# Optimization experiments

Measured on AMD Instinct MI355X. Metric: run time of the kernel, lower is better.

The kernel has to match this reference:

```python
import jax, jax.numpy as jnp
import numpy as np

N_NODES = 32768
N_EDGES = 524288
N_FEAT = 256
HID = 256
N_GRAPHS = 64
N_CLASSES = 4
NODES_PER_GRAPH = N_NODES // N_GRAPHS
BN_EPS = 1e-5


def setup_inputs() -> dict:
    key = jax.random.key(0)
    ks = jax.random.split(key, 16)
    x = jax.random.normal(ks[0], (N_NODES, N_FEAT), dtype=jnp.float32)
    edge_index = jax.random.randint(ks[1], (2, N_EDGES), 0, N_NODES, dtype=jnp.int32)
    batch = (jnp.arange(N_NODES, dtype=jnp.int32) // NODES_PER_GRAPH)
    def xavier(k, shape):
        fan_in, fan_out = shape[0], shape[1]
        a = float(np.sqrt(6.0 / (fan_in + fan_out)))
        return jax.random.uniform(k, shape, jnp.float32, -a, a)
    return {
        "x": x, "edge_index": edge_index, "batch": batch,
        "W1": xavier(ks[2], (N_FEAT, HID)), "b1": jnp.zeros((HID,), jnp.float32),
        "g1": jnp.ones((HID,), jnp.float32), "be1": jnp.zeros((HID,), jnp.float32),
        "W2": xavier(ks[3], (HID, HID)), "b2": jnp.zeros((HID,), jnp.float32),
        "g2": jnp.ones((HID,), jnp.float32), "be2": jnp.zeros((HID,), jnp.float32),
        "W_ih": xavier(ks[4], (HID, 4 * HID)), "W_hh": xavier(ks[5], (HID, 4 * HID)),
        "b_ih": jnp.zeros((4 * HID,), jnp.float32), "b_hh": jnp.zeros((4 * HID,), jnp.float32),
        "W_fc": xavier(ks[6], (HID, N_CLASSES)), "b_fc": jnp.zeros((N_CLASSES,), jnp.float32),
    }


def gcn_conv(x, W, b, src, dst):
    # PyG GCNConv: add self-loops, symmetric normalization, aggregate, then bias
    h = x @ W                                   # [N, H]
    deg = jnp.zeros((x.shape[0],), h.dtype).at[dst].add(1.0) + 1.0  # in-deg + self-loop
    dinv = jax.lax.rsqrt(deg)
    coef = dinv[src] * dinv[dst]                # [E]
    msg = h[src] * coef[:, None]                # gather + scale, [E, H]
    agg = jnp.zeros_like(h).at[dst].add(msg)    # scatter-add
    agg = agg + h * (1.0 / deg)[:, None]        # self-loop term (norm = 1/deg)
    return agg + b


def batch_norm(x, gamma, beta):
    mean = jnp.mean(x, axis=0)
    var = jnp.mean(jnp.square(x - mean), axis=0)  # biased, as torch BN training
    return (x - mean) * jax.lax.rsqrt(var + BN_EPS) * gamma + beta


def reference(x, edge_index, batch, W1, b1, g1, be1, W2, b2, g2, be2,
              W_ih, W_hh, b_ih, b_hh, W_fc, b_fc):
    src, dst = edge_index[0], edge_index[1]
    h = jax.nn.relu(batch_norm(gcn_conv(x, W1, b1, src, dst), g1, be1))
    h = jax.nn.relu(batch_norm(gcn_conv(h, W2, b2, src, dst), g2, be2))
    # global mean pool over graphs
    sums = jax.ops.segment_sum(h, batch, num_segments=N_GRAPHS)
    cnts = jax.ops.segment_sum(jnp.ones((h.shape[0],), h.dtype), batch, num_segments=N_GRAPHS)
    pooled = sums / cnts[:, None]               # [G, H]
    # LSTM, seq_len = 1, zero initial state -> single cell step
    h0 = jnp.zeros((N_GRAPHS, HID), h.dtype)
    c0 = jnp.zeros((N_GRAPHS, HID), h.dtype)
    gates = pooled @ W_ih + h0 @ W_hh + b_ih + b_hh  # [G, 4H]
    i, f, g, o = jnp.split(gates, 4, axis=1)
    c1 = jax.nn.sigmoid(f) * c0 + jax.nn.sigmoid(i) * jnp.tanh(g)
    h1 = jax.nn.sigmoid(o) * jnp.tanh(c1)
    logits = h1 @ W_fc + b_fc
    logp = jax.nn.log_softmax(logits, axis=1)
    return (logp, (h1[None], c1[None]))
```

## Files before the change

### kernel.cpp

```cpp
#include <hip/hip_runtime.h>
#include <math.h>

#define N_NODES 32768
#define N_FEAT 256
#define HID 256
#define N_GRAPHS 64
#define NPG 512
#define N_CLASSES 4
#define BN_EPS 1e-5f

typedef __attribute__((ext_vector_type(8))) short bf16x8;
typedef __attribute__((ext_vector_type(4))) float f32x4;

__device__ __forceinline__ ushort f2b(float f) {
    union { float f; uint u; } v; v.f = f;
    uint u = v.u;
    return (ushort)((u + 0x7FFFu + ((u >> 16) & 1u)) >> 16);
}
__device__ __forceinline__ float bf2f(ushort u) {
    union { uint u; float f; } v; v.u = ((uint)u) << 16;
    return v.f;
}

__global__ void k_count(const int* __restrict__ dst, int* __restrict__ degcnt, int E) {
    int e = blockIdx.x * 256 + threadIdx.x;
    if (e < E) atomicAdd(&degcnt[dst[e]], 1);
}

__global__ __launch_bounds__(1024) void k_scan_all(const int* __restrict__ degcnt,
                                                   float* __restrict__ dinv,
                                                   int* __restrict__ row_start,
                                                   int* __restrict__ cursor) {
    __shared__ int wsum[16];
    int t = threadIdx.x;
    int base = t * 32;
    int s = 0;
#pragma unroll
    for (int i = 0; i < 32; ++i) s += degcnt[base + i];
    int lane = t & 63, w = t >> 6;
    int v = s;
    for (int off = 1; off < 64; off <<= 1) {
        int u = __shfl_up(v, off);
        if (lane >= off) v += u;
    }
    if (lane == 63) wsum[w] = v;
    __syncthreads();
    if (t < 16) {
        int x = wsum[t];
        for (int off = 1; off < 16; off <<= 1) {
            int u = __shfl_up(x, off, 16);
            if (t >= off) x += u;
        }
        wsum[t] = x;
    }
    __syncthreads();
    int run = ((w > 0) ? wsum[w - 1] : 0) + v - s;
    for (int i = 0; i < 32; ++i) {
        int n = base + i;
        int c = degcnt[n];
        row_start[n] = run;
        cursor[n] = run;
        dinv[n] = rsqrtf((float)(c + 1));
        run += c;
    }
}

__global__ void k_fill(const int* __restrict__ src, const int* __restrict__ dst,
                       const float* __restrict__ dinv, int* __restrict__ cursor,
                       uint2* __restrict__ csr, int E) {
    int e = blockIdx.x * 256 + threadIdx.x;
    if (e >= E) return;
    int d = dst[e], s = src[e];
    float coef = dinv[s] * dinv[d];
    int pos = atomicAdd(&cursor[d], 1);
    csr[pos] = make_uint2((uint)s, __float_as_uint(coef));
}

__global__ void k_prep(const float* __restrict__ x, ushort* __restrict__ xb, int n8blk,
                       const float* __restrict__ W1, const float* __restrict__ W2,
                       ushort* __restrict__ Wt1, ushort* __restrict__ Wt2) {
    int b = blockIdx.x;
    if (b < n8blk) {
        int i = b * 256 + threadIdx.x;
        float4 v0 = *(const float4*)(x + (size_t)i * 8);
        float4 v1 = *(const float4*)(x + (size_t)i * 8 + 4);
        uint4 o;
        o.x = (uint)f2b(v0.x) | ((uint)f2b(v0.y) << 16);
        o.y = (uint)f2b(v0.z) | ((uint)f2b(v0.w) << 16);
        o.z = (uint)f2b(v1.x) | ((uint)f2b(v1.y) << 16);
        o.w = (uint)f2b(v1.z) | ((uint)f2b(v1.w) << 16);
        *(uint4*)(xb + (size_t)i * 8) = o;
    } else {
        int wb = b - n8blk;
        const float* W = (wb < 256) ? W1 : W2;
        ushort* Wt = (wb < 256) ? Wt1 : Wt2;
        int n = wb & 255;
        int k = threadIdx.x;
        Wt[n * 256 + k] = f2b(W[k * 256 + n]);
    }
}

__global__ __launch_bounds__(256) void k_gemm_bf16(const ushort* __restrict__ A,
                                                   const ushort* __restrict__ Bt,
                                                   ushort* __restrict__ hs) {
    int wid = threadIdx.x >> 6;
    int lane = threadIdx.x & 63;
    int m0 = blockIdx.y * 256 + wid * 64;
    int n0 = blockIdx.x * 64;
    int r = lane & 15;
    int ko = (lane >> 4) * 8;

    const ushort* Ab = A + (size_t)(m0 + r) * 256 + ko;
    const ushort* Bb = Bt + (size_t)(n0 + r) * 256 + ko;

    f32x4 acc[4][4] = {};
#pragma unroll
    for (int ks = 0; ks < 8; ++ks) {
        bf16x8 a[4], b[4];
#pragma unroll
        for (int i = 0; i < 4; ++i) {
            a[i] = *(const bf16x8*)(Ab + i * (16 * 256) + ks * 32);
            b[i] = *(const bf16x8*)(Bb + i * (16 * 256) + ks * 32);
        }
#pragma unroll
        for (int i = 0; i < 4; ++i)
#pragma unroll
            for (int j = 0; j < 4; ++j)
                acc[i][j] = __builtin_amdgcn_mfma_f32_16x16x32_bf16(a[i], b[j], acc[i][j], 0, 0, 0);
    }

    int rr = (lane >> 4) * 4;
    int cc = lane & 15;
#pragma unroll
    for (int i = 0; i < 4; ++i) {
        int row = m0 + i * 16 + rr;
#pragma unroll
        for (int j = 0; j < 4; ++j) {
            int col = n0 + j * 16 + cc;
            int slice = col >> 5;
            int within = col & 31;
            ushort* dstp = hs + (size_t)slice * (N_NODES * 32) + (size_t)row * 32 + within;
#pragma unroll
            for (int r2 = 0; r2 < 4; ++r2)
                dstp[(size_t)r2 * 32] = f2b(acc[i][j][r2]);
        }
    }
}

__global__ __launch_bounds__(256) void k_agg_bn(const ushort* __restrict__ hs,
                                                const uint2* __restrict__ csr,
                                                const int* __restrict__ row_start,
                                                const int* __restrict__ degcnt,
                                                const float* __restrict__ dinv,
                                                const float* __restrict__ bias,
                                                float* __restrict__ agg,
                                                float* __restrict__ bnsum,
                                                float* __restrict__ bnsq) {
    int slice = blockIdx.x & 7;
    int grp = blockIdx.x >> 3;
    int wid = threadIdx.x >> 6;
    int lane = threadIdx.x & 63;
    int j4 = lane >> 4;
    int fp = lane & 15;
    const ushort* hS = hs + (size_t)slice * (N_NODES * 32);

    float b0 = 0.f, b1v = 0.f;
    if (j4 == 0) {
        b0 = bias[slice * 32 + fp * 2];
        b1v = bias[slice * 32 + fp * 2 + 1];
    }

    float s0 = 0.f, q0 = 0.f, s1 = 0.f, q1 = 0.f;

    for (int t = 0; t < 8; ++t) {
        int n = grp * 32 + wid * 8 + t;
        int base = row_start[n];
        int cnt = degcnt[n];
        float ax = 0.f, ay = 0.f;
        if (j4 == 0) {
            float dv = dinv[n];
            uint hv = *(const uint*)(hS + (size_t)n * 32 + fp * 2);
            float inv = dv * dv;
            ax = bf2f((ushort)hv) * inv + b0;
            ay = bf2f((ushort)(hv >> 16)) * inv + b1v;
        }
        int j = j4;
        for (; j + 4 < cnt; j += 8) {
            uint2 e0 = csr[base + j];
            uint2 e1 = csr[base + j + 4];
            float c0 = __uint_as_float(e0.y);
            float c1 = __uint_as_float(e1.y);
            uint h0 = *(const uint*)(hS + (size_t)e0.x * 32 + fp * 2);
            uint h1 = *(const uint*)(hS + (size_t)e1.x * 32 + fp * 2);
            ax += c0 * bf2f((ushort)h0) + c1 * bf2f((ushort)h1);
            ay += c0 * bf2f((ushort)(h0 >> 16)) + c1 * bf2f((ushort)(h1 >> 16));
        }
        if (j < cnt) {
            uint2 e0 = csr[base + j];
            float c0 = __uint_as_float(e0.y);
            uint h0 = *(const uint*)(hS + (size_t)e0.x * 32 + fp * 2);
            ax += c0 * bf2f((ushort)h0);
            ay += c0 * bf2f((ushort)(h0 >> 16));
        }
        ax += __shfl_xor(ax, 16); ay += __shfl_xor(ay, 16);
        ax += __shfl_xor(ax, 32); ay += __shfl_xor(ay, 32);
        if (j4 == 0) {
            *(float2*)&agg[(size_t)n * HID + slice * 32 + fp * 2] = make_float2(ax, ay);
            s0 += ax; q0 += ax * ax; s1 += ay; q1 += ay * ay;
        }
    }

    __shared__ float ls[4][16][4];
    if (j4 == 0) {
        ls[wid][fp][0] = s0; ls[wid][fp][1] = q0;
        ls[wid][fp][2] = s1; ls[wid][fp][3] = q1;
    }
    __syncthreads();
    if (threadIdx.x < 64) {
        int f = threadIdx.x >> 2, v = threadIdx.x & 3;
        float tsum = ls[0][f][v] + ls[1][f][v] + ls[2][f][v] + ls[3][f][v];
        int feat = slice * 32 + f * 2 + (v >> 1);
        if ((v & 1) == 0) atomicAdd(&bnsum[feat], tsum);
        else              atomicAdd(&bnsq[feat], tsum);
    }
}

__global__ void k_bn_apply_b(const float* __restrict__ x, const float* __restrict__ bnsum,
                             const float* __restrict__ bnsq, const float* __restrict__ gamma,
                             const float* __restrict__ beta, ushort* __restrict__ out) {
    int i = blockIdx.x * 256 + threadIdx.x;
    if (i >= N_NODES * HID / 4) return;
    int f = (i & 63) * 4;
    const float invN = 1.0f / (float)N_NODES;
    float4 v = *(const float4*)(x + (size_t)i * 4);
    float r[4];
    float vv[4] = {v.x, v.y, v.z, v.w};
#pragma unroll
    for (int q = 0; q < 4; ++q) {
        float mean = bnsum[f + q] * invN;
        float var = bnsq[f + q] * invN - mean * mean;
        float t = (vv[q] - mean) * rsqrtf(var + BN_EPS) * gamma[f + q] + beta[f + q];
        r[q] = t > 0.0f ? t : 0.0f;
    }
    uint2 o;
    o.x = (uint)f2b(r[0]) | ((uint)f2b(r[1]) << 16);
    o.y = (uint)f2b(r[2]) | ((uint)f2b(r[3]) << 16);
    *(uint2*)(out + (size_t)i * 4) = o;
}

__global__ __launch_bounds__(256) void k_bn_pool(const float* __restrict__ agg,
                                                 const float* __restrict__ bnsum,
                                                 const float* __restrict__ bnsq,
                                                 const float* __restrict__ gamma,
                                                 const float* __restrict__ beta,
                                                 float* __restrict__ pooled) {
    int g = blockIdx.x >> 4;
    int blk = blockIdx.x & 15;
    int f = threadIdx.x;
    const float invN = 1.0f / (float)N_NODES;
    float mean = bnsum[f] * invN;
    float var = bnsq[f] * invN - mean * mean;
    float sc = rsqrtf(var + BN_EPS) * gamma[f];
    float sh = beta[f] - mean * sc;
    int r0 = g * NPG + blk * 32;
    float s = 0.0f;
#pragma unroll 4
    for (int r = 0; r < 32; ++r) {
        float v = agg[(size_t)(r0 + r) * HID + f] * sc + sh;
        s += v > 0.0f ? v : 0.0f;
    }
    atomicAdd(&pooled[g * HID + f], s);
}

__global__ __launch_bounds__(256) void k_head(const float* __restrict__ pooled,
                                              const float* __restrict__ W_ih,
                                              const float* __restrict__ b_ih,
                                              const float* __restrict__ b_hh,
                                              const float* __restrict__ W_fc,
                                              const float* __restrict__ b_fc,
                                              float* __restrict__ out) {
    __shared__ float p[HID];
    __shared__ float lsum[N_CLASSES][256];
    __shared__ float logits[N_CLASSES];
    int g = blockIdx.x, j = threadIdx.x;
    p[j] = pooled[g * HID + j] * (1.0f / (float)NPG);
    __syncthreads();

    float gi = 0.f, gf = 0.f, gg = 0.f, go = 0.f;
#pragma unroll 4
    for (int k = 0; k < HID; ++k) {
        float pk = p[k];
        const float* w = &W_ih[(size_t)k * (4 * HID) + j];
        gi += pk * w[0];
        gf += pk * w[HID];
        gg += pk * w[2 * HID];
        go += pk * w[3 * HID];
    }
    gi += b_ih[j] + b_hh[j];
    gf += b_ih[HID + j] + b_hh[HID + j];
    gg += b_ih[2 * HID + j] + b_hh[2 * HID + j];
    go += b_ih[3 * HID + j] + b_hh[3 * HID + j];
    (void)gf;

    float si = 1.f / (1.f + expf(-gi));
    float so = 1.f / (1.f + expf(-go));
    float c1 = si * tanhf(gg);
    float h1 = so * tanhf(c1);

    out[N_GRAPHS * N_CLASSES + g * HID + j] = h1;
    out[N_GRAPHS * N_CLASSES + N_GRAPHS * HID + g * HID + j] = c1;

#pragma unroll
    for (int c = 0; c < N_CLASSES; ++c)
        lsum[c][j] = h1 * W_fc[j * N_CLASSES + c];
    __syncthreads();
    for (int s = 128; s > 0; s >>= 1) {
        if (j < s) {
#pragma unroll
            for (int c = 0; c < N_CLASSES; ++c)
                lsum[c][j] += lsum[c][j + s];
        }
        __syncthreads();
    }
    if (j < N_CLASSES) logits[j] = lsum[j][0] + b_fc[j];
    __syncthreads();
    if (j < N_CLASSES) {
        float m = fmaxf(fmaxf(logits[0], logits[1]), fmaxf(logits[2], logits[3]));
        float lse = m + logf(expf(logits[0] - m) + expf(logits[1] - m) +
                             expf(logits[2] - m) + expf(logits[3] - m));
        out[g * N_CLASSES + j] = logits[j] - lse;
    }
}

extern "C" void kernel_launch(void* const* d_in, const int* in_sizes, int n_in,
                              void* d_out, int out_size, void* d_ws, size_t ws_size,
                              hipStream_t stream) {
    const float* x    = (const float*)d_in[0];
    const int*   ei   = (const int*)d_in[1];
    const float* W1   = (const float*)d_in[3];
    const float* b1   = (const float*)d_in[4];
    const float* g1   = (const float*)d_in[5];
    const float* be1  = (const float*)d_in[6];
    const float* W2   = (const float*)d_in[7];
    const float* b2   = (const float*)d_in[8];
    const float* g2   = (const float*)d_in[9];
    const float* be2  = (const float*)d_in[10];
    const float* W_ih = (const float*)d_in[11];
    const float* b_ih = (const float*)d_in[13];
    const float* b_hh = (const float*)d_in[14];
    const float* W_fc = (const float*)d_in[15];
    const float* b_fc = (const float*)d_in[16];
    float* out = (float*)d_out;

    int E = in_sizes[1] / 2;
    const int* src = ei;
    const int* dst = ei + E;

    const size_t MAT = (size_t)N_NODES * HID;
    float*  agg  = (float*)d_ws;
    ushort* xb   = (ushort*)(agg + MAT);
    ushort* hs   = xb + MAT;
    ushort* Wt1  = hs + MAT;
    ushort* Wt2  = Wt1 + 65536;
    float*  dinv = (float*)(Wt2 + 65536);
    int*    row_start = (int*)(dinv + N_NODES);
    int*    cursor    = row_start + N_NODES;
    uint2*  csr       = (uint2*)(cursor + N_NODES);
    int*    degcnt = (int*)(csr + E);
    float*  bn1sum = (float*)(degcnt + N_NODES);
    float*  bn1sq  = bn1sum + HID;
    float*  bn2sum = bn1sq + HID;
    float*  bn2sq  = bn2sum + HID;
    float*  pooled = bn2sq + HID;
    size_t zeroBytes = (size_t)N_NODES * 4 + 4 * HID * 4 + (size_t)N_GRAPHS * HID * 4;

    dim3 blk(256);
    int edgeBlocks = (E + 255) / 256;
    int n8blk = (int)(MAT / 8 / 256);
    int vec4Blocks = (int)(MAT / 4 / 256);
    dim3 gemmGrid(HID / 64, N_NODES / 256);

    hipMemsetAsync(degcnt, 0, zeroBytes, stream);

    k_count<<<edgeBlocks, blk, 0, stream>>>(dst, degcnt, E);
    k_scan_all<<<1, dim3(1024), 0, stream>>>(degcnt, dinv, row_start, cursor);
    k_fill<<<edgeBlocks, blk, 0, stream>>>(src, dst, dinv, cursor, csr, E);
    k_prep<<<n8blk + 512, blk, 0, stream>>>(x, xb, n8blk, W1, W2, Wt1, Wt2);

    k_gemm_bf16<<<gemmGrid, blk, 0, stream>>>(xb, Wt1, hs);
    k_agg_bn<<<8192, blk, 0, stream>>>(hs, csr, row_start, degcnt, dinv, b1, agg, bn1sum, bn1sq);
    k_bn_apply_b<<<vec4Blocks, blk, 0, stream>>>(agg, bn1sum, bn1sq, g1, be1, xb);

    k_gemm_bf16<<<gemmGrid, blk, 0, stream>>>(xb, Wt2, hs);
    k_agg_bn<<<8192, blk, 0, stream>>>(hs, csr, row_start, degcnt, dinv, b2, agg, bn2sum, bn2sq);
    k_bn_pool<<<N_GRAPHS * 16, blk, 0, stream>>>(agg, bn2sum, bn2sq, g2, be2, pooled);

    k_head<<<N_GRAPHS, blk, 0, stream>>>(pooled, W_ih, b_ih, b_hh, W_fc, b_fc, out);
}
```

Measured before the change: 343.8 us.

## Factor GCN normalization into GEMM epilogue and drop per-edge coefficients

Rewrites the symmetric normalization: the GEMM epilogue scales each row by dinv[src], and aggregation applies dinv[dst] once per node, so the CSR stores only source indices (4 bytes instead of 8 per edge). The aggregation kernel now uses 8 lanes per 32-feature slice, each loading 4 bf16 values (8 bytes), with 8 edge streams per wave instead of 4. The aim is to cut edge-list traffic and per-edge multiplies and to widen gathers. Trade-offs: the pre-scaled h is rounded to bf16 after scaling, and there is an extra shuffle level plus a dinv load in the GEMM epilogue.

```diff
diff --git a/kernel.cpp b/kernel.cpp
--- a/kernel.cpp
+++ b/kernel.cpp
@@ -17,8 +17,12 @@
     uint u = v.u;
     return (ushort)((u + 0x7FFFu + ((u >> 16) & 1u)) >> 16);
 }
-__device__ __forceinline__ float bf2f(ushort u) {
-    union { uint u; float f; } v; v.u = ((uint)u) << 16;
+__device__ __forceinline__ float bflo(uint u) {
+    union { uint u; float f; } v; v.u = u << 16;
+    return v.f;
+}
+__device__ __forceinline__ float bfhi(uint u) {
+    union { uint u; float f; } v; v.u = u & 0xFFFF0000u;
     return v.f;
 }
 
@@ -66,14 +70,12 @@
 }
 
 __global__ void k_fill(const int* __restrict__ src, const int* __restrict__ dst,
-                       const float* __restrict__ dinv, int* __restrict__ cursor,
-                       uint2* __restrict__ csr, int E) {
+                       int* __restrict__ cursor, uint* __restrict__ csrs, int E) {
     int e = blockIdx.x * 256 + threadIdx.x;
     if (e >= E) return;
-    int d = dst[e], s = src[e];
-    float coef = dinv[s] * dinv[d];
+    int d = dst[e];
     int pos = atomicAdd(&cursor[d], 1);
-    csr[pos] = make_uint2((uint)s, __float_as_uint(coef));
+    csrs[pos] = (uint)src[e];
 }
 
 __global__ void k_prep(const float* __restrict__ x, ushort* __restrict__ xb, int n8blk,
@@ -102,6 +104,7 @@
 
 __global__ __launch_bounds__(256) void k_gemm_bf16(const ushort* __restrict__ A,
                                                    const ushort* __restrict__ Bt,
+                                                   const float* __restrict__ dinv,
                                                    ushort* __restrict__ hs) {
     int wid = threadIdx.x >> 6;
     int lane = threadIdx.x & 63;
@@ -135,20 +138,22 @@
     for (int i = 0; i < 4; ++i) {
         int row = m0 + i * 16 + rr;
 #pragma unroll
-        for (int j = 0; j < 4; ++j) {
-            int col = n0 + j * 16 + cc;
-            int slice = col >> 5;
-            int within = col & 31;
-            ushort* dstp = hs + (size_t)slice * (N_NODES * 32) + (size_t)row * 32 + within;
-#pragma unroll
-            for (int r2 = 0; r2 < 4; ++r2)
-                dstp[(size_t)r2 * 32] = f2b(acc[i][j][r2]);
+        for (int r2 = 0; r2 < 4; ++r2) {
+            float dv = dinv[row + r2];
+#pragma unroll
+            for (int j = 0; j < 4; ++j) {
+                int col = n0 + j * 16 + cc;
+                int slice = col >> 5;
+                int within = col & 31;
+                hs[(size_t)slice * (N_NODES * 32) + (size_t)(row + r2) * 32 + within] =
+                    f2b(acc[i][j][r2] * dv);
+            }
         }
     }
 }
 
 __global__ __launch_bounds__(256) void k_agg_bn(const ushort* __restrict__ hs,
-                                                const uint2* __restrict__ csr,
+                                                const uint* __restrict__ csrs,
                                                 const int* __restrict__ row_start,
                                                 const int* __restrict__ degcnt,
                                                 const float* __restrict__ dinv,
@@ -160,66 +165,77 @@
     int grp = blockIdx.x >> 3;
     int wid = threadIdx.x >> 6;
     int lane = threadIdx.x & 63;
-    int j4 = lane >> 4;
-    int fp = lane & 15;
+    int j8 = lane >> 3;
+    int fp = lane & 7;
     const ushort* hS = hs + (size_t)slice * (N_NODES * 32);
 
-    float b0 = 0.f, b1v = 0.f;
-    if (j4 == 0) {
-        b0 = bias[slice * 32 + fp * 2];
-        b1v = bias[slice * 32 + fp * 2 + 1];
-    }
-
-    float s0 = 0.f, q0 = 0.f, s1 = 0.f, q1 = 0.f;
+    float b0 = 0.f, b1 = 0.f, b2 = 0.f, b3 = 0.f;
+    if (j8 == 0) {
+        b0 = bias[slice * 32 + fp * 4 + 0];
+        b1 = bias[slice * 32 + fp * 4 + 1];
+        b2 = bias[slice * 32 + fp * 4 + 2];
+        b3 = bias[slice * 32 + fp * 4 + 3];
+    }
+
+    float st[8] = {0.f, 0.f, 0.f, 0.f, 0.f, 0.f, 0.f, 0.f};
 
     for (int t = 0; t < 8; ++t) {
         int n = grp * 32 + wid * 8 + t;
+        float dv = dinv[n];
         int base = row_start[n];
         int cnt = degcnt[n];
-        float ax = 0.f, ay = 0.f;
-        if (j4 == 0) {
-            float dv = dinv[n];
-            uint hv = *(const uint*)(hS + (size_t)n * 32 + fp * 2);
-            float inv = dv * dv;
-            ax = bf2f((ushort)hv) * inv + b0;
-            ay = bf2f((ushort)(hv >> 16)) * inv + b1v;
-        }
-        int j = j4;
-        for (; j + 4 < cnt; j += 8) {
-            uint2 e0 = csr[base + j];
-            uint2 e1 = csr[base + j + 4];
-            float c0 = __uint_as_float(e0.y);
-            float c1 = __uint_as_float(e1.y);
-            uint h0 = *(const uint*)(hS + (size_t)e0.x * 32 + fp * 2);
-            uint h1 = *(const uint*)(hS + (size_t)e1.x * 32 + fp * 2);
-            ax += c0 * bf2f((ushort)h0) + c1 * bf2f((ushort)h1);
-            ay += c0 * bf2f((ushort)(h0 >> 16)) + c1 * bf2f((ushort)(h1 >> 16));
+        float a0 = 0.f, a1 = 0.f, a2 = 0.f, a3 = 0.f;
+        if (j8 == 0) {
+            uint2 hv = *(const uint2*)(hS + (size_t)n * 32 + fp * 4);
+            a0 = bflo(hv.x); a1 = bfhi(hv.x);
+            a2 = bflo(hv.y); a3 = bfhi(hv.y);
+        }
+        int j = j8;
+        for (; j + 8 < cnt; j += 16) {
+            uint s0 = csrs[base + j];
+            uint s1 = csrs[base + j + 8];
+            uint2 h0 = *(const uint2*)(hS + (size_t)s0 * 32 + fp * 4);
+            uint2 h1 = *(const uint2*)(hS + (size_t)s1 * 32 + fp * 4);
+            a0 += bflo(h0.x) + bflo(h1.x);
+            a1 += bfhi(h0.x) + bfhi(h1.x);
+            a2 += bflo(h0.y) + bflo(h1.y);
+            a3 += bfhi(h0.y) + bfhi(h1.y);
         }
         if (j < cnt) {
-            uint2 e0 = csr[base + j];
-            float c0 = __uint_as_float(e0.y);
-            uint h0 = *(const uint*)(hS + (size_t)e0.x * 32 + fp * 2);
-            ax += c0 * bf2f((ushort)h0);
-            ay += c0 * bf2f((ushort)(h0 >> 16));
-        }
-        ax += __shfl_xor(ax, 16); ay += __shfl_xor(ay, 16);
-        ax += __shfl_xor(ax, 32); ay += __shfl_xor(ay, 32);
-        if (j4 == 0) {
-            *(float2*)&agg[(size_t)n * HID + slice * 32 + fp * 2] = make_float2(ax, ay);
-            s0 += ax; q0 += ax * ax; s1 += ay; q1 += ay * ay;
-        }
-    }
-
-    __shared__ float ls[4][16][4];
-    if (j4 == 0) {
-        ls[wid][fp][0] = s0; ls[wid][fp][1] = q0;
-        ls[wid][fp][2] = s1; ls[wid][fp][3] = q1;
+            uint s0 = csrs[base + j];
+            uint2 h0 = *(const uint2*)(hS + (size_t)s0 * 32 + fp * 4);
+            a0 += bflo(h0.x); a1 += bfhi(h0.x);
+            a2 += bflo(h0.y); a3 += bfhi(h0.y);
+        }
+        a0 += __shfl_xor(a0, 8);  a1 += __shfl_xor(a1, 8);
+        a2 += __shfl_xor(a2, 8);  a3 += __shfl_xor(a3, 8);
+        a0 += __shfl_xor(a0, 16); a1 += __shfl_xor(a1, 16);
+        a2 += __shfl_xor(a2, 16); a3 += __shfl_xor(a3, 16);
+        a0 += __shfl_xor(a0, 32); a1 += __shfl_xor(a1, 32);
+        a2 += __shfl_xor(a2, 32); a3 += __shfl_xor(a3, 32);
+        if (j8 == 0) {
+            float o0 = a0 * dv + b0;
+            float o1 = a1 * dv + b1;
+            float o2 = a2 * dv + b2;
+            float o3 = a3 * dv + b3;
+            *(float4*)&agg[(size_t)n * HID + slice * 32 + fp * 4] = make_float4(o0, o1, o2, o3);
+            st[0] += o0; st[1] += o0 * o0;
+            st[2] += o1; st[3] += o1 * o1;
+            st[4] += o2; st[5] += o2 * o2;
+            st[6] += o3; st[7] += o3 * o3;
+        }
+    }
+
+    __shared__ float ls[4][8][8];
+    if (j8 == 0) {
+#pragma unroll
+        for (int v = 0; v < 8; ++v) ls[wid][fp][v] = st[v];
     }
     __syncthreads();
     if (threadIdx.x < 64) {
-        int f = threadIdx.x >> 2, v = threadIdx.x & 3;
+        int f = threadIdx.x >> 3, v = threadIdx.x & 7;
         float tsum = ls[0][f][v] + ls[1][f][v] + ls[2][f][v] + ls[3][f][v];
-        int feat = slice * 32 + f * 2 + (v >> 1);
+        int feat = slice * 32 + f * 4 + (v >> 1);
         if ((v & 1) == 0) atomicAdd(&bnsum[feat], tsum);
         else              atomicAdd(&bnsq[feat], tsum);
     }
@@ -365,8 +381,8 @@
     float*  dinv = (float*)(Wt2 + 65536);
     int*    row_start = (int*)(dinv + N_NODES);
     int*    cursor    = row_start + N_NODES;
-    uint2*  csr       = (uint2*)(cursor + N_NODES);
-    int*    degcnt = (int*)(csr + E);
+    uint*   csrs      = (uint*)(cursor + N_NODES);
+    int*    degcnt = (int*)(csrs + E);
     float*  bn1sum = (float*)(degcnt + N_NODES);
     float*  bn1sq  = bn1sum + HID;
     float*  bn2sum = bn1sq + HID;
@@ -384,15 +400,15 @@
 
     k_count<<<edgeBlocks, blk, 0, stream>>>(dst, degcnt, E);
     k_scan_all<<<1, dim3(1024), 0, stream>>>(degcnt, dinv, row_start, cursor);
-    k_fill<<<edgeBlocks, blk, 0, stream>>>(src, dst, dinv, cursor, csr, E);
+    k_fill<<<edgeBlocks, blk, 0, stream>>>(src, dst, cursor, csrs, E);
     k_prep<<<n8blk + 512, blk, 0, stream>>>(x, xb, n8blk, W1, W2, Wt1, Wt2);
 
-    k_gemm_bf16<<<gemmGrid, blk, 0, stream>>>(xb, Wt1, hs);
-    k_agg_bn<<<8192, blk, 0, stream>>>(hs, csr, row_start, degcnt, dinv, b1, agg, bn1sum, bn1sq);
+    k_gemm_bf16<<<gemmGrid, blk, 0, stream>>>(xb, Wt1, dinv, hs);
+    k_agg_bn<<<8192, blk, 0, stream>>>(hs, csrs, row_start, degcnt, dinv, b1, agg, bn1sum, bn1sq);
     k_bn_apply_b<<<vec4Blocks, blk, 0, stream>>>(agg, bn1sum, bn1sq, g1, be1, xb);
 
-    k_gemm_bf16<<<gemmGrid, blk, 0, stream>>>(xb, Wt2, hs);
-    k_agg_bn<<<8192, blk, 0, stream>>>(hs, csr, row_start, degcnt, dinv, b2, agg, bn2sum, bn2sq);
+    k_gemm_bf16<<<gemmGrid, blk, 0, stream>>>(xb, Wt2, dinv, hs);
+    k_agg_bn<<<8192, blk, 0, stream>>>(hs, csrs, row_start, degcnt, dinv, b2, agg, bn2sum, bn2sq);
     k_bn_pool<<<N_GRAPHS * 16, blk, 0, stream>>>(agg, bn2sum, bn2sq, g2, be2, pooled);
 
     k_head<<<N_GRAPHS, blk, 0, stream>>>(pooled, W_ih, b_ih, b_hh, W_fc, b_fc, out);
```

Measured after the change: 309.5 us. 10.0% less time.
